# Optimization experiments

Hardware: AMD Instinct MI355X
Metric: run time of the kernel (lower is better)

## Reference

```python
import jax, jax.numpy as jnp
import numpy as np

N_PER_G = 100  # nodes per graph


def setup_inputs() -> dict:
    key = jax.random.key(0)
    ks = jax.random.split(key, 12)
    N, G, E = 100000, 1000, 1600000
    ninp, nout, K, H, H2 = 3, 10, 5, 64, 32
    x = jax.random.normal(ks[0], (N, ninp), jnp.float32)
    # within-graph random edges (contiguous node blocks per graph)
    epg = E // G
    gid = jnp.arange(E, dtype=jnp.int32) // epg
    src = jax.random.randint(ks[1], (E,), 0, N_PER_G, jnp.int32) + gid * N_PER_G
    dst = jax.random.randint(ks[2], (E,), 0, N_PER_G, jnp.int32) + gid * N_PER_G
    edge_index = jnp.stack([src, dst])
    batch = (jnp.arange(N, dtype=jnp.int32) // N_PER_G)
    lambda_max = 1.5 + 0.5 * jax.random.uniform(ks[3], (G,), jnp.float32)
    s = 0.05
    W1 = jax.random.normal(ks[4], (K, ninp, H), jnp.float32) * s
    b1 = jnp.zeros((H,), jnp.float32)
    W2 = jax.random.normal(ks[5], (K, H, H), jnp.float32) * s
    b2 = jnp.zeros((H,), jnp.float32)
    W3 = jax.random.normal(ks[6], (K, H, H), jnp.float32) * s
    b3 = jnp.zeros((H,), jnp.float32)
    bn_gamma = jnp.ones((H,), jnp.float32)
    bn_beta = jnp.zeros((H,), jnp.float32)
    bn_mean = jnp.zeros((H,), jnp.float32)
    bn_var = jnp.ones((H,), jnp.float32)
    fc1_w = jax.random.normal(ks[7], (H, H2), jnp.float32) * s
    fc1_b = jnp.zeros((H2,), jnp.float32)
    fc2_w = jax.random.normal(ks[8], (H2, nout), jnp.float32) * s
    fc2_b = jnp.zeros((nout,), jnp.float32)
    return dict(x=x, edge_index=edge_index, batch=batch, lambda_max=lambda_max,
                W1=W1, b1=b1, W2=W2, b2=b2, W3=W3, b3=b3,
                bn_gamma=bn_gamma, bn_beta=bn_beta, bn_mean=bn_mean, bn_var=bn_var,
                fc1_w=fc1_w, fc1_b=fc1_b, fc2_w=fc2_w, fc2_b=fc2_b)


def _cheb_conv(x, W, b, row, col, coef_edge, coef_loop):
    # PyG ChebConv with sym-normalized scaled Laplacian:
    # Lhat x = scatter_add(coef_edge * x[col] -> row) + coef_loop * x
    N = x.shape[0]
    def lhat(h):
        return jax.ops.segment_sum(coef_edge[:, None] * h[col], row,
                                   num_segments=N) + coef_loop[:, None] * h
    Tx0 = x
    out = Tx0 @ W[0]
    Tx1 = lhat(x)
    out = out + Tx1 @ W[1]
    for k in range(2, W.shape[0]):
        Tx2 = 2.0 * lhat(Tx1) - Tx0
        out = out + Tx2 @ W[k]
        Tx0, Tx1 = Tx1, Tx2
    return out + b


def reference(x, edge_index, batch, lambda_max,
              W1, b1, W2, b2, W3, b3,
              bn_gamma, bn_beta, bn_mean, bn_var,
              fc1_w, fc1_b, fc2_w, fc2_b):
    N = x.shape[0]
    G = lambda_max.shape[0]
    row, col = edge_index[0], edge_index[1]
    # sym Laplacian normalization, scaled by 2/lambda_max (per-graph)
    deg = jax.ops.segment_sum(jnp.ones_like(row, dtype=x.dtype), row, num_segments=N)
    dis = jnp.where(deg > 0, deg, 1.0) ** -0.5
    dis = jnp.where(deg > 0, dis, 0.0)
    lmax_e = lambda_max[batch[row]]
    coef_edge = -(2.0 / lmax_e) * dis[row] * dis[col]   # off-diagonal of Lhat
    coef_loop = 2.0 / lambda_max[batch] - 1.0           # diagonal of Lhat
    h = jax.nn.relu(_cheb_conv(x, W1, b1, row, col, coef_edge, coef_loop))
    h = jax.nn.relu(_cheb_conv(h, W2, b2, row, col, coef_edge, coef_loop))
    h = jax.nn.relu(_cheb_conv(h, W3, b3, row, col, coef_edge, coef_loop))
    # global mean pool over graphs
    sums = jax.ops.segment_sum(h, batch, num_segments=G)
    cnts = jax.ops.segment_sum(jnp.ones((N,), h.dtype), batch, num_segments=G)
    g = sums / jnp.maximum(cnts, 1.0)[:, None]
    # BatchNorm1d (eval mode, running stats), eps=1e-5
    g = (g - bn_mean) * jax.lax.rsqrt(bn_var + 1e-5) * bn_gamma + bn_beta
    g = jax.nn.relu(g @ fc1_w + fc1_b)
    return jax.nn.log_softmax(g @ fc2_w + fc2_b, axis=1)
```

## Files before the change

kernel.cpp:

```cpp
#include <hip/hip_runtime.h>

#define NPG 100
#define HF 64
#define NROW 128
#define ST 72
#define SAT 136
#define CMW 28

typedef float  f4   __attribute__((ext_vector_type(4)));
typedef float  f16v __attribute__((ext_vector_type(16)));
typedef short  bf8  __attribute__((ext_vector_type(8)));

#define SZ_TC  (HF * SAT * 2)
#define SZ_TRM (NROW * ST * 2)
#define OFF_TC  0
#define OFF_TRM SZ_TC
#define OFF_CM  0
#define OFF_MISC (OFF_TRM + SZ_TRM)
#define SMEM_BYTES (OFF_MISC + 1280)

#define WT_TOTAL 46080

__device__ __forceinline__ unsigned short f2bf(float f) {
    unsigned u = __float_as_uint(f);
    u += 0x7fffu + ((u >> 16) & 1u);
    return (unsigned short)(u >> 16);
}
__device__ __forceinline__ unsigned cvt_pk_bf16(float lo, float hi) {
    unsigned r;
    asm("v_cvt_pk_bf16_f32 %0, %1, %2" : "=v"(r) : "v"(lo), "v"(hi));
    return r;
}
__device__ __forceinline__ f16v zerov16() {
    f16v z;
    #pragma unroll
    for (int i = 0; i < 16; i++) z[i] = 0.f;
    return z;
}

union BF8U { unsigned u[4]; bf8 b; };

__global__ void wconv(const float* __restrict__ W1, const float* __restrict__ W2,
                      const float* __restrict__ W3, unsigned short* __restrict__ ws)
{
    int idx = blockIdx.x * 256 + threadIdx.x;
    if (idx >= WT_TOTAL) return;
    float v;
    if (idx < 5120) {
        int k5 = idx >> 10, rem = idx & 1023, fo = rem >> 4, fi = rem & 15;
        v = (fi < 3) ? W1[(k5 * 3 + fi) * HF + fo] : 0.f;
    } else if (idx < 25600) {
        int j = idx - 5120;
        int k5 = j >> 12, rem = j & 4095, fo = rem >> 6, fi = rem & 63;
        v = W2[(k5 * HF + fi) * HF + fo];
    } else {
        int j = idx - 25600;
        int k5 = j >> 12, rem = j & 4095, fo = rem >> 6, fi = rem & 63;
        v = W3[(k5 * HF + fi) * HF + fo];
    }
    ws[idx] = f2bf(v);
}

__launch_bounds__(256, 2)
__global__ void chebreg(const float* __restrict__ x, const int* __restrict__ ei,
                        const float* __restrict__ lambda_max,
                        const unsigned short* __restrict__ Wt,
                        const float* __restrict__ b1, const float* __restrict__ b2,
                        const float* __restrict__ b3,
                        const float* __restrict__ bng, const float* __restrict__ bnb,
                        const float* __restrict__ bnm, const float* __restrict__ bnv,
                        const float* __restrict__ fc1w, const float* __restrict__ fc1b,
                        const float* __restrict__ fc2w, const float* __restrict__ fc2b,
                        float* __restrict__ out, int E_total, int epg)
{
    extern __shared__ char sm[];
    const int tid = threadIdx.x;
    const int g = blockIdx.x;
    const int ebase = g * epg, nbase = g * NPG;
    const int wg = tid >> 6, lane = tid & 63;
    const int l31 = lane & 31, hh = lane >> 5;
    const int ht  = wg & 1;
    const int Mt0 = (wg >> 1) * 2;
    const int fo  = ht * 32 + l31;

    unsigned* Cm  = (unsigned*)(sm + OFF_CM);
    float* dis    = (float*)(sm + OFF_MISC);
    float* pool   = (float*)(sm + OFF_MISC + 448);
    float* gvn    = (float*)(sm + OFF_MISC + 704);
    float* zf     = (float*)(sm + OFF_MISC + 960);
    float* logits = (float*)(sm + OFF_MISC + 1088);
    float* lsep   = (float*)(sm + OFF_MISC + 1152);

    const float lam = lambda_max[g];
    const float two_l = 2.0f / lam;
    const float cl = two_l - 1.0f;

    for (int i = tid; i < (NROW * CMW) / 4; i += 256)
        ((f4*)Cm)[i] = (f4){0.f, 0.f, 0.f, 0.f};
    __syncthreads();
    for (int e = tid; e < epg; e += 256) {
        int r = ei[ebase + e] - nbase;
        int c = ei[E_total + ebase + e] - nbase;
        atomicAdd(&Cm[r * CMW + (c >> 2)], 1u << (8 * (c & 3)));
    }
    __syncthreads();
    if (tid < 112) {
        float dv = 0.f;
        if (tid < NPG) {
            unsigned s = 0;
            #pragma unroll
            for (int w = 0; w < CMW; w++) {
                unsigned u = Cm[tid * CMW + w];
                s += (u & 255) + ((u >> 8) & 255) + ((u >> 16) & 255) + (u >> 24);
            }
            dv = s > 0 ? rsqrtf((float)s) : 0.f;
        }
        dis[tid] = dv;
    }
    __syncthreads();

    bf8 af[2][7];
    #pragma unroll
    for (int m = 0; m < 2; m++) {
        int rr = 32 * (Mt0 + m) + l31;
        bool rv = (rr < NPG);
        float base = rv ? (-two_l * dis[rr]) : 0.f;
        #pragma unroll
        for (int Ks = 0; Ks < 7; Ks++) {
            int k0 = Ks * 16 + 8 * hh;
            unsigned w0 = rv ? Cm[rr * CMW + (k0 >> 2)]     : 0u;
            unsigned w1 = rv ? Cm[rr * CMW + (k0 >> 2) + 1] : 0u;
            float vv[8];
            #pragma unroll
            for (int j = 0; j < 8; j++) {
                int k = k0 + j;
                unsigned cnt = (((j < 4) ? w0 : w1) >> (8 * (k & 3))) & 255u;
                float v = base * (float)cnt * dis[k];
                if (rv && k == rr) v += cl;
                vv[j] = v;
            }
            BF8U t;
            #pragma unroll
            for (int p = 0; p < 4; p++) t.u[p] = cvt_pk_bf16(vv[2 * p], vv[2 * p + 1]);
            af[m][Ks] = t.b;
        }
    }
    __syncthreads();

    for (int i = tid; i < (SZ_TC + SZ_TRM) / 16; i += 256)
        ((f4*)sm)[i] = (f4){0.f, 0.f, 0.f, 0.f};
    if (tid < HF) pool[tid] = 0.f;
    __syncthreads();
    if (tid < NPG) {
        unsigned short h0 = f2bf(x[(nbase + tid) * 3 + 0]);
        unsigned short h1 = f2bf(x[(nbase + tid) * 3 + 1]);
        unsigned short h2 = f2bf(x[(nbase + tid) * 3 + 2]);
        *(unsigned*)(sm + OFF_TRM + (tid * ST) * 2) = (unsigned)h0 | ((unsigned)h1 << 16);
        *(unsigned short*)(sm + OFF_TRM + (tid * ST + 2) * 2) = h2;
        *(unsigned short*)(sm + OFF_TC + (0 * SAT + tid) * 2) = h0;
        *(unsigned short*)(sm + OFF_TC + (1 * SAT + tid) * 2) = h1;
        *(unsigned short*)(sm + OFF_TC + (2 * SAT + tid) * 2) = h2;
    }
    __syncthreads();

    f16v acc[2];
    unsigned prev[2][8], oldr[2][8];
    const float* bsv[3] = {b1, b2, b3};

    for (int L = 0; L < 3; L++) {
        const bool l1 = (L == 0);
        const unsigned short* Wl = l1 ? Wt : (Wt + (L == 1 ? 5120 : 25600));
        acc[0] = zerov16();
        acc[1] = zerov16();

        if (L == 0) {
            #pragma unroll
            for (int m = 0; m < 2; m++) {
                unsigned short tv[16];
                #pragma unroll
                for (int r = 0; r < 16; r++) {
                    int np = (Mt0 + m) * 32 + (r & 3) + 8 * (r >> 2) + 4 * hh;
                    tv[r] = *(const unsigned short*)(sm + OFF_TRM + (np * ST + fo) * 2);
                }
                #pragma unroll
                for (int p = 0; p < 8; p++)
                    prev[m][p] = (unsigned)tv[2 * p] | ((unsigned)tv[2 * p + 1] << 16);
            }
        }

        auto TW = [&](int k5) {
            const int nKs = l1 ? 1 : 4;
            for (int Ks = 0; Ks < nKs; Ks++) {
                bf8 bw;
                if (l1) bw = *(const bf8*)(Wl + (k5 * 64 + fo) * 16 + 8 * hh);
                else    bw = *(const bf8*)(Wl + (k5 * 64 + fo) * 64 + Ks * 16 + 8 * hh);
                #pragma unroll
                for (int m = 0; m < 2; m++) {
                    bf8 a = *(const bf8*)(sm + OFF_TRM +
                              (((Mt0 + m) * 32 + l31) * ST + Ks * 16 + 8 * hh) * 2);
                    acc[m] = __builtin_amdgcn_mfma_f32_32x32x16_bf16(a, bw, acc[m], 0, 0, 0);
                }
            }
        };

        TW(0);
        for (int s = 1; s <= 4; s++) {
            bf8 bfr[7];
            #pragma unroll
            for (int Ks = 0; Ks < 7; Ks++)
                bfr[Ks] = *(const bf8*)(sm + OFF_TC +
                            (fo * SAT + Ks * 16 + 8 * hh) * 2);
            __syncthreads();
            #pragma unroll
            for (int m = 0; m < 2; m++) {
                f16v c = zerov16();
                #pragma unroll
                for (int Ks = 0; Ks < 7; Ks++)
                    c = __builtin_amdgcn_mfma_f32_32x32x16_bf16(af[m][Ks], bfr[Ks], c, 0, 0, 0);
                #pragma unroll
                for (int p = 0; p < 8; p++) {
                    float ve = c[2 * p], vo = c[2 * p + 1];
                    if (s >= 2) {
                        unsigned o = oldr[m][p];
                        ve = 2.f * ve - __uint_as_float(o << 16);
                        vo = 2.f * vo - __uint_as_float(o & 0xffff0000u);
                    }
                    oldr[m][p] = prev[m][p];
                    prev[m][p] = cvt_pk_bf16(ve, vo);
                }
                #pragma unroll
                for (int q4 = 0; q4 < 4; q4++) {
                    int np0 = (Mt0 + m) * 32 + 8 * q4 + 4 * hh;
                    uint2 pk;
                    pk.x = prev[m][2 * q4];
                    pk.y = prev[m][2 * q4 + 1];
                    *(uint2*)(sm + OFF_TC + (fo * SAT + np0) * 2) = pk;
                }
                #pragma unroll
                for (int p = 0; p < 8; p++) {
                    int r0 = 2 * p;
                    int npb = (Mt0 + m) * 32 + (r0 & 3) + 8 * (r0 >> 2) + 4 * hh;
                    char* ad = sm + OFF_TRM + (npb * ST + fo) * 2;
                    *(unsigned short*)ad = (unsigned short)prev[m][p];
                    *(unsigned short*)(ad + ST * 2) = (unsigned short)(prev[m][p] >> 16);
                }
            }
            __syncthreads();
            TW(s);
        }
        __syncthreads();

        const float bias = bsv[L][fo];
        if (L < 2) {
            #pragma unroll
            for (int m = 0; m < 2; m++) {
                #pragma unroll
                for (int p = 0; p < 8; p++) {
                    float ve = fmaxf(acc[m][2 * p]     + bias, 0.f);
                    float vo = fmaxf(acc[m][2 * p + 1] + bias, 0.f);
                    prev[m][p] = cvt_pk_bf16(ve, vo);
                }
                #pragma unroll
                for (int q4 = 0; q4 < 4; q4++) {
                    int np0 = (Mt0 + m) * 32 + 8 * q4 + 4 * hh;
                    uint2 pk;
                    pk.x = prev[m][2 * q4];
                    pk.y = prev[m][2 * q4 + 1];
                    *(uint2*)(sm + OFF_TC + (fo * SAT + np0) * 2) = pk;
                }
                #pragma unroll
                for (int p = 0; p < 8; p++) {
                    int r0 = 2 * p;
                    int npb = (Mt0 + m) * 32 + (r0 & 3) + 8 * (r0 >> 2) + 4 * hh;
                    char* ad = sm + OFF_TRM + (npb * ST + fo) * 2;
                    *(unsigned short*)ad = (unsigned short)prev[m][p];
                    *(unsigned short*)(ad + ST * 2) = (unsigned short)(prev[m][p] >> 16);
                }
            }
            __syncthreads();
        } else {
            float ssum = 0.f;
            #pragma unroll
            for (int m = 0; m < 2; m++) {
                #pragma unroll
                for (int r = 0; r < 16; r++) {
                    int np = (Mt0 + m) * 32 + (r & 3) + 8 * (r >> 2) + 4 * hh;
                    float h = fmaxf(acc[m][r] + bias, 0.f);
                    if (np < NPG) ssum += h;
                }
            }
            ssum += __shfl_xor(ssum, 32, 64);
            if (hh == 0) atomicAdd(&pool[fo], ssum);
            __syncthreads();
        }
    }

    if (tid < HF) {
        float gv = pool[tid] * (1.0f / NPG);
        gv = (gv - bnm[tid]) * rsqrtf(bnv[tid] + 1e-5f) * bng[tid] + bnb[tid];
        gvn[tid] = gv;
    }
    __syncthreads();
    if (tid < 32) {
        float a = fc1b[tid];
        for (int f = 0; f < HF; f++) a += gvn[f] * fc1w[f * 32 + tid];
        zf[tid] = fmaxf(a, 0.f);
    }
    __syncthreads();
    if (tid < 10) {
        float a = fc2b[tid];
        for (int k = 0; k < 32; k++) a += zf[k] * fc2w[k * 10 + tid];
        logits[tid] = a;
    }
    __syncthreads();
    if (tid == 0) {
        float m = logits[0];
        for (int i = 1; i < 10; i++) m = fmaxf(m, logits[i]);
        float s = 0.f;
        for (int i = 0; i < 10; i++) s += expf(logits[i] - m);
        lsep[0] = m + logf(s);
    }
    __syncthreads();
    if (tid < 10) out[g * 10 + tid] = logits[tid] - lsep[0];
}

extern "C" void kernel_launch(void* const* d_in, const int* in_sizes, int n_in,
                              void* d_out, int out_size, void* d_ws, size_t ws_size,
                              hipStream_t stream) {
    const float* x    = (const float*)d_in[0];
    const int*   ei   = (const int*)d_in[1];
    const float* lmax = (const float*)d_in[3];
    const float* W1   = (const float*)d_in[4];
    const float* b1   = (const float*)d_in[5];
    const float* W2   = (const float*)d_in[6];
    const float* b2   = (const float*)d_in[7];
    const float* W3   = (const float*)d_in[8];
    const float* b3   = (const float*)d_in[9];
    const float* bng  = (const float*)d_in[10];
    const float* bnb  = (const float*)d_in[11];
    const float* bnm  = (const float*)d_in[12];
    const float* bnv  = (const float*)d_in[13];
    const float* fc1w = (const float*)d_in[14];
    const float* fc1b = (const float*)d_in[15];
    const float* fc2w = (const float*)d_in[16];
    const float* fc2b = (const float*)d_in[17];

    const int E = in_sizes[1] / 2;
    const int G = in_sizes[3];
    const int epg = E / G;

    unsigned short* Wt = (unsigned short*)d_ws;

    wconv<<<(WT_TOTAL + 255) / 256, 256, 0, stream>>>(W1, W2, W3, Wt);

    hipFuncSetAttribute((const void*)chebreg,
                        hipFuncAttributeMaxDynamicSharedMemorySize, SMEM_BYTES);

    chebreg<<<G, 256, SMEM_BYTES, stream>>>(x, ei, lmax, Wt, b1, b2, b3,
                                            bng, bnb, bnm, bnv, fc1w, fc1b, fc2w, fc2b,
                                            (float*)d_out, E, epg);
}
```

Before: 164.2 us.

## Restructure Chebyshev recurrence to node-major waves with register-resident T operands

Each wave now owns a 32-node slab and computes Lhat·T in transposed form, keeping the resulting T_k tiles in registers and feeding them to the weight MFMA through v_permlane32_swap. This drops the second row-major LDS copy of T. The T buffer is double-buffered so only one barrier is needed per recurrence step, and layer 1 skips the unused 32-feature half. Biases are staged in LDS, and pooling is a plain LDS reduction instead of atomics. The cost is more register pressure, two-byte scattered LDS stores, and a larger LDS footprint from the double buffer, which could reduce occupancy.

```diff
diff --git a/kernel.cpp b/kernel.cpp
--- a/kernel.cpp
+++ b/kernel.cpp
@@ -2,22 +2,17 @@
 
 #define NPG 100
 #define HF 64
-#define NROW 128
-#define ST 72
 #define SAT 136
-#define CMW 28
+#define CMW 29
 
 typedef float  f4   __attribute__((ext_vector_type(4)));
 typedef float  f16v __attribute__((ext_vector_type(16)));
 typedef short  bf8  __attribute__((ext_vector_type(8)));
 
-#define SZ_TC  (HF * SAT * 2)
-#define SZ_TRM (NROW * ST * 2)
-#define OFF_TC  0
-#define OFF_TRM SZ_TC
-#define OFF_CM  0
-#define OFF_MISC (OFF_TRM + SZ_TRM)
-#define SMEM_BYTES (OFF_MISC + 1280)
+#define NB_T  (HF * SAT * 2)
+#define OFF_MISC (2 * NB_T)
+#define MISC_BYTES 2048
+#define SMEM_BYTES (OFF_MISC + MISC_BYTES)
 
 #define WT_TOTAL 46080
 
@@ -79,23 +74,23 @@
     const int ebase = g * epg, nbase = g * NPG;
     const int wg = tid >> 6, lane = tid & 63;
     const int l31 = lane & 31, hh = lane >> 5;
-    const int ht  = wg & 1;
-    const int Mt0 = (wg >> 1) * 2;
-    const int fo  = ht * 32 + l31;
-
-    unsigned* Cm  = (unsigned*)(sm + OFF_CM);
+    const int nb = 32 * wg;
+    const int np = nb + l31;
+    const bool npv = (np < NPG);
+
+    unsigned* Cm  = (unsigned*)sm;
     float* dis    = (float*)(sm + OFF_MISC);
-    float* pool   = (float*)(sm + OFF_MISC + 448);
-    float* gvn    = (float*)(sm + OFF_MISC + 704);
-    float* zf     = (float*)(sm + OFF_MISC + 960);
-    float* logits = (float*)(sm + OFF_MISC + 1088);
-    float* lsep   = (float*)(sm + OFF_MISC + 1152);
+    float* b_all  = (float*)(sm + OFF_MISC + 448);
+    float* gvn    = (float*)(sm + OFF_MISC + 1216);
+    float* zf     = (float*)(sm + OFF_MISC + 1472);
+    float* logits = (float*)(sm + OFF_MISC + 1600);
+    float* lsep   = (float*)(sm + OFF_MISC + 1664);
 
     const float lam = lambda_max[g];
     const float two_l = 2.0f / lam;
     const float cl = two_l - 1.0f;
 
-    for (int i = tid; i < (NROW * CMW) / 4; i += 256)
+    for (int i = tid; i < (128 * CMW) / 4; i += 256)
         ((f4*)Cm)[i] = (f4){0.f, 0.f, 0.f, 0.f};
     __syncthreads();
     for (int e = tid; e < epg; e += 256) {
@@ -109,7 +104,7 @@
         if (tid < NPG) {
             unsigned s = 0;
             #pragma unroll
-            for (int w = 0; w < CMW; w++) {
+            for (int w = 0; w < 25; w++) {
                 unsigned u = Cm[tid * CMW + w];
                 s += (u & 255) + ((u >> 8) & 255) + ((u >> 16) & 255) + (u >> 24);
             }
@@ -117,190 +112,213 @@
         }
         dis[tid] = dv;
     }
-    __syncthreads();
-
-    bf8 af[2][7];
-    #pragma unroll
-    for (int m = 0; m < 2; m++) {
-        int rr = 32 * (Mt0 + m) + l31;
-        bool rv = (rr < NPG);
-        float base = rv ? (-two_l * dis[rr]) : 0.f;
+    if (tid < 192)
+        b_all[tid] = (tid < 64) ? b1[tid] : (tid < 128) ? b2[tid - 64] : b3[tid - 128];
+    __syncthreads();
+
+    bf8 afT[7];
+    {
+        float base = npv ? (-two_l * dis[np]) : 0.f;
         #pragma unroll
         for (int Ks = 0; Ks < 7; Ks++) {
-            int k0 = Ks * 16 + 8 * hh;
-            unsigned w0 = rv ? Cm[rr * CMW + (k0 >> 2)]     : 0u;
-            unsigned w1 = rv ? Cm[rr * CMW + (k0 >> 2) + 1] : 0u;
+            int n0 = Ks * 16 + 8 * hh;
+            unsigned w0 = npv ? Cm[np * CMW + (n0 >> 2)]     : 0u;
+            unsigned w1 = npv ? Cm[np * CMW + (n0 >> 2) + 1] : 0u;
             float vv[8];
             #pragma unroll
             for (int j = 0; j < 8; j++) {
-                int k = k0 + j;
-                unsigned cnt = (((j < 4) ? w0 : w1) >> (8 * (k & 3))) & 255u;
-                float v = base * (float)cnt * dis[k];
-                if (rv && k == rr) v += cl;
+                int n = n0 + j;
+                unsigned cnt = (((j < 4) ? w0 : w1) >> (8 * (n & 3))) & 255u;
+                float v = base * (float)cnt * dis[n];
+                if (npv && n == np) v += cl;
                 vv[j] = v;
             }
             BF8U t;
             #pragma unroll
             for (int p = 0; p < 4; p++) t.u[p] = cvt_pk_bf16(vv[2 * p], vv[2 * p + 1]);
-            af[m][Ks] = t.b;
+            afT[Ks] = t.b;
         }
     }
     __syncthreads();
 
-    for (int i = tid; i < (SZ_TC + SZ_TRM) / 16; i += 256)
+    for (int i = tid; i < (2 * NB_T) / 16; i += 256)
         ((f4*)sm)[i] = (f4){0.f, 0.f, 0.f, 0.f};
-    if (tid < HF) pool[tid] = 0.f;
-    __syncthreads();
-    if (tid < NPG) {
-        unsigned short h0 = f2bf(x[(nbase + tid) * 3 + 0]);
-        unsigned short h1 = f2bf(x[(nbase + tid) * 3 + 1]);
-        unsigned short h2 = f2bf(x[(nbase + tid) * 3 + 2]);
-        *(unsigned*)(sm + OFF_TRM + (tid * ST) * 2) = (unsigned)h0 | ((unsigned)h1 << 16);
-        *(unsigned short*)(sm + OFF_TRM + (tid * ST + 2) * 2) = h2;
-        *(unsigned short*)(sm + OFF_TC + (0 * SAT + tid) * 2) = h0;
-        *(unsigned short*)(sm + OFF_TC + (1 * SAT + tid) * 2) = h1;
-        *(unsigned short*)(sm + OFF_TC + (2 * SAT + tid) * 2) = h2;
+    __syncthreads();
+
+    unsigned prev[2][8], oldr[2][8];
+    #pragma unroll
+    for (int ct = 0; ct < 2; ct++)
+        #pragma unroll
+        for (int p = 0; p < 8; p++) prev[ct][p] = 0u;
+
+    if (hh == 0 && npv) {
+        float x0 = x[(nbase + np) * 3 + 0];
+        float x1 = x[(nbase + np) * 3 + 1];
+        float x2 = x[(nbase + np) * 3 + 2];
+        prev[0][0] = cvt_pk_bf16(x0, x1);
+        prev[0][1] = cvt_pk_bf16(x2, 0.f);
+        *(unsigned short*)(sm + (0 * SAT + np) * 2) = (unsigned short)(prev[0][0] & 0xffff);
+        *(unsigned short*)(sm + (1 * SAT + np) * 2) = (unsigned short)(prev[0][0] >> 16);
+        *(unsigned short*)(sm + (2 * SAT + np) * 2) = (unsigned short)(prev[0][1] & 0xffff);
     }
     __syncthreads();
 
     f16v acc[2];
-    unsigned prev[2][8], oldr[2][8];
-    const float* bsv[3] = {b1, b2, b3};
+    int cur = 0;
 
     for (int L = 0; L < 3; L++) {
-        const bool l1 = (L == 0);
-        const unsigned short* Wl = l1 ? Wt : (Wt + (L == 1 ? 5120 : 25600));
+        const bool l0 = (L == 0);
+        const unsigned short* Wl = l0 ? Wt : (Wt + (L == 1 ? 5120 : 25600));
+        const int wstr = l0 ? 16 : 64;
+        const int nKs  = l0 ? 1 : 4;
         acc[0] = zerov16();
         acc[1] = zerov16();
 
-        if (L == 0) {
-            #pragma unroll
-            for (int m = 0; m < 2; m++) {
-                unsigned short tv[16];
-                #pragma unroll
-                for (int r = 0; r < 16; r++) {
-                    int np = (Mt0 + m) * 32 + (r & 3) + 8 * (r >> 2) + 4 * hh;
-                    tv[r] = *(const unsigned short*)(sm + OFF_TRM + (np * ST + fo) * 2);
-                }
-                #pragma unroll
-                for (int p = 0; p < 8; p++)
-                    prev[m][p] = (unsigned)tv[2 * p] | ((unsigned)tv[2 * p + 1] << 16);
-            }
-        }
-
-        auto TW = [&](int k5) {
-            const int nKs = l1 ? 1 : 4;
-            for (int Ks = 0; Ks < nKs; Ks++) {
-                bf8 bw;
-                if (l1) bw = *(const bf8*)(Wl + (k5 * 64 + fo) * 16 + 8 * hh);
-                else    bw = *(const bf8*)(Wl + (k5 * 64 + fo) * 64 + Ks * 16 + 8 * hh);
-                #pragma unroll
-                for (int m = 0; m < 2; m++) {
-                    bf8 a = *(const bf8*)(sm + OFF_TRM +
-                              (((Mt0 + m) * 32 + l31) * ST + Ks * 16 + 8 * hh) * 2);
-                    acc[m] = __builtin_amdgcn_mfma_f32_32x32x16_bf16(a, bw, acc[m], 0, 0, 0);
+        auto TWreg = [&](int k5) {
+            #pragma unroll
+            for (int Ks = 0; Ks < 4; Ks++) {
+                if (Ks < nKs) {
+                    unsigned a0 = prev[Ks >> 1][4 * (Ks & 1) + 0];
+                    unsigned b0 = prev[Ks >> 1][4 * (Ks & 1) + 2];
+                    unsigned a1 = prev[Ks >> 1][4 * (Ks & 1) + 1];
+                    unsigned b1v = prev[Ks >> 1][4 * (Ks & 1) + 3];
+                    asm volatile("v_permlane32_swap_b32 %0, %1" : "+v"(a0), "+v"(b0));
+                    asm volatile("v_permlane32_swap_b32 %0, %1" : "+v"(a1), "+v"(b1v));
+                    BF8U bfr; bfr.u[0] = a0; bfr.u[1] = a1; bfr.u[2] = b0; bfr.u[3] = b1v;
+                    #pragma unroll
+                    for (int ct = 0; ct < 2; ct++) {
+                        bf8 wf = *(const bf8*)(Wl + (k5 * 64 + 32 * ct + l31) * wstr
+                                               + Ks * 16 + 8 * hh);
+                        acc[ct] = __builtin_amdgcn_mfma_f32_32x32x16_bf16(wf, bfr.b, acc[ct], 0, 0, 0);
+                    }
                 }
             }
         };
 
-        TW(0);
         for (int s = 1; s <= 4; s++) {
-            bf8 bfr[7];
+            const char* bcur = sm + cur * NB_T;
+            bf8 Af0[7], Af1[7];
             #pragma unroll
             for (int Ks = 0; Ks < 7; Ks++)
-                bfr[Ks] = *(const bf8*)(sm + OFF_TC +
-                            (fo * SAT + Ks * 16 + 8 * hh) * 2);
-            __syncthreads();
-            #pragma unroll
-            for (int m = 0; m < 2; m++) {
-                f16v c = zerov16();
+                Af0[Ks] = *(const bf8*)(bcur + ((0 + l31) * SAT + Ks * 16 + 8 * hh) * 2);
+            if (!l0) {
                 #pragma unroll
                 for (int Ks = 0; Ks < 7; Ks++)
-                    c = __builtin_amdgcn_mfma_f32_32x32x16_bf16(af[m][Ks], bfr[Ks], c, 0, 0, 0);
+                    Af1[Ks] = *(const bf8*)(bcur + ((32 + l31) * SAT + Ks * 16 + 8 * hh) * 2);
+            }
+            f16v c0 = zerov16(), c1 = zerov16();
+            #pragma unroll
+            for (int Ks = 0; Ks < 7; Ks++)
+                c0 = __builtin_amdgcn_mfma_f32_32x32x16_bf16(Af0[Ks], afT[Ks], c0, 0, 0, 0);
+            if (!l0) {
+                #pragma unroll
+                for (int Ks = 0; Ks < 7; Ks++)
+                    c1 = __builtin_amdgcn_mfma_f32_32x32x16_bf16(Af1[Ks], afT[Ks], c1, 0, 0, 0);
+            }
+
+            TWreg(s - 1);
+
+            #pragma unroll
+            for (int p = 0; p < 8; p++) {
+                float ve = c0[2 * p], vo = c0[2 * p + 1];
+                if (s >= 2) {
+                    unsigned o = oldr[0][p];
+                    ve = 2.f * ve - __uint_as_float(o << 16);
+                    vo = 2.f * vo - __uint_as_float(o & 0xffff0000u);
+                }
+                oldr[0][p] = prev[0][p];
+                prev[0][p] = cvt_pk_bf16(ve, vo);
+            }
+            if (!l0) {
                 #pragma unroll
                 for (int p = 0; p < 8; p++) {
-                    float ve = c[2 * p], vo = c[2 * p + 1];
+                    float ve = c1[2 * p], vo = c1[2 * p + 1];
                     if (s >= 2) {
-                        unsigned o = oldr[m][p];
+                        unsigned o = oldr[1][p];
                         ve = 2.f * ve - __uint_as_float(o << 16);
                         vo = 2.f * vo - __uint_as_float(o & 0xffff0000u);
                     }
-                    oldr[m][p] = prev[m][p];
-                    prev[m][p] = cvt_pk_bf16(ve, vo);
-                }
-                #pragma unroll
-                for (int q4 = 0; q4 < 4; q4++) {
-                    int np0 = (Mt0 + m) * 32 + 8 * q4 + 4 * hh;
-                    uint2 pk;
-                    pk.x = prev[m][2 * q4];
-                    pk.y = prev[m][2 * q4 + 1];
-                    *(uint2*)(sm + OFF_TC + (fo * SAT + np0) * 2) = pk;
-                }
+                    oldr[1][p] = prev[1][p];
+                    prev[1][p] = cvt_pk_bf16(ve, vo);
+                }
+            }
+
+            if (s < 4) {
+                char* bnx = sm + (cur ^ 1) * NB_T;
+                if (l0) {
+                    if (hh == 0) {
+                        *(unsigned short*)(bnx + (0 * SAT + np) * 2) = (unsigned short)(prev[0][0] & 0xffff);
+                        *(unsigned short*)(bnx + (1 * SAT + np) * 2) = (unsigned short)(prev[0][0] >> 16);
+                        *(unsigned short*)(bnx + (2 * SAT + np) * 2) = (unsigned short)(prev[0][1] & 0xffff);
+                    }
+                } else {
+                    #pragma unroll
+                    for (int ct = 0; ct < 2; ct++) {
+                        #pragma unroll
+                        for (int p = 0; p < 8; p++) {
+                            int fo = 32 * ct + ((2 * p) & 3) + 8 * (p >> 1) + 4 * hh;
+                            *(unsigned short*)(bnx + (fo * SAT + np) * 2)       = (unsigned short)(prev[ct][p] & 0xffff);
+                            *(unsigned short*)(bnx + ((fo + 1) * SAT + np) * 2) = (unsigned short)(prev[ct][p] >> 16);
+                        }
+                    }
+                }
+            }
+            __syncthreads();
+            cur ^= 1;
+        }
+
+        TWreg(4);
+
+        if (L < 2) {
+            const float* bl = b_all + L * 64;
+            char* bt0 = sm + cur * NB_T;
+            #pragma unroll
+            for (int ct = 0; ct < 2; ct++) {
                 #pragma unroll
                 for (int p = 0; p < 8; p++) {
-                    int r0 = 2 * p;
-                    int npb = (Mt0 + m) * 32 + (r0 & 3) + 8 * (r0 >> 2) + 4 * hh;
-                    char* ad = sm + OFF_TRM + (npb * ST + fo) * 2;
-                    *(unsigned short*)ad = (unsigned short)prev[m][p];
-                    *(unsigned short*)(ad + ST * 2) = (unsigned short)(prev[m][p] >> 16);
-                }
-            }
-            __syncthreads();
-            TW(s);
-        }
-        __syncthreads();
-
-        const float bias = bsv[L][fo];
-        if (L < 2) {
-            #pragma unroll
-            for (int m = 0; m < 2; m++) {
-                #pragma unroll
-                for (int p = 0; p < 8; p++) {
-                    float ve = fmaxf(acc[m][2 * p]     + bias, 0.f);
-                    float vo = fmaxf(acc[m][2 * p + 1] + bias, 0.f);
-                    prev[m][p] = cvt_pk_bf16(ve, vo);
-                }
-                #pragma unroll
-                for (int q4 = 0; q4 < 4; q4++) {
-                    int np0 = (Mt0 + m) * 32 + 8 * q4 + 4 * hh;
-                    uint2 pk;
-                    pk.x = prev[m][2 * q4];
-                    pk.y = prev[m][2 * q4 + 1];
-                    *(uint2*)(sm + OFF_TC + (fo * SAT + np0) * 2) = pk;
-                }
-                #pragma unroll
-                for (int p = 0; p < 8; p++) {
-                    int r0 = 2 * p;
-                    int npb = (Mt0 + m) * 32 + (r0 & 3) + 8 * (r0 >> 2) + 4 * hh;
-                    char* ad = sm + OFF_TRM + (npb * ST + fo) * 2;
-                    *(unsigned short*)ad = (unsigned short)prev[m][p];
-                    *(unsigned short*)(ad + ST * 2) = (unsigned short)(prev[m][p] >> 16);
+                    int fo = 32 * ct + ((2 * p) & 3) + 8 * (p >> 1) + 4 * hh;
+                    float2 bb = *(const float2*)(bl + fo);
+                    float ve = fmaxf(acc[ct][2 * p]     + bb.x, 0.f);
+                    float vo = fmaxf(acc[ct][2 * p + 1] + bb.y, 0.f);
+                    prev[ct][p] = cvt_pk_bf16(ve, vo);
+                    *(unsigned short*)(bt0 + (fo * SAT + np) * 2)       = (unsigned short)(prev[ct][p] & 0xffff);
+                    *(unsigned short*)(bt0 + ((fo + 1) * SAT + np) * 2) = (unsigned short)(prev[ct][p] >> 16);
                 }
             }
             __syncthreads();
         } else {
-            float ssum = 0.f;
-            #pragma unroll
-            for (int m = 0; m < 2; m++) {
-                #pragma unroll
-                for (int r = 0; r < 16; r++) {
-                    int np = (Mt0 + m) * 32 + (r & 3) + 8 * (r >> 2) + 4 * hh;
-                    float h = fmaxf(acc[m][r] + bias, 0.f);
-                    if (np < NPG) ssum += h;
-                }
-            }
-            ssum += __shfl_xor(ssum, 32, 64);
-            if (hh == 0) atomicAdd(&pool[fo], ssum);
+            float* Sc = (float*)sm;
+            const float* bl = b_all + 128;
+            #pragma unroll
+            for (int ct = 0; ct < 2; ct++) {
+                #pragma unroll
+                for (int p = 0; p < 8; p++) {
+                    int fo = 32 * ct + ((2 * p) & 3) + 8 * (p >> 1) + 4 * hh;
+                    float2 bb = *(const float2*)(bl + fo);
+                    float ve = fmaxf(acc[ct][2 * p]     + bb.x, 0.f);
+                    float vo = fmaxf(acc[ct][2 * p + 1] + bb.y, 0.f);
+                    if (npv) {
+                        Sc[fo * 132 + np]       = ve;
+                        Sc[(fo + 1) * 132 + np] = vo;
+                    }
+                }
+            }
+            __syncthreads();
+            if (tid < HF) {
+                float ssum = 0.f;
+                #pragma unroll
+                for (int k = 0; k < 25; k++) {
+                    f4 v = *(const f4*)(Sc + tid * 132 + 4 * k);
+                    ssum += v[0] + v[1] + v[2] + v[3];
+                }
+                float gv = ssum * (1.0f / NPG);
+                gv = (gv - bnm[tid]) * rsqrtf(bnv[tid] + 1e-5f) * bng[tid] + bnb[tid];
+                gvn[tid] = gv;
+            }
             __syncthreads();
         }
     }
 
-    if (tid < HF) {
-        float gv = pool[tid] * (1.0f / NPG);
-        gv = (gv - bnm[tid]) * rsqrtf(bnv[tid] + 1e-5f) * bng[tid] + bnb[tid];
-        gvn[tid] = gv;
-    }
-    __syncthreads();
     if (tid < 32) {
         float a = fc1b[tid];
         for (int f = 0; f < HF; f++) a += gvn[f] * fc1w[f * 32 + tid];
```

After: 181.5 us. 1.11x slower.

## Double-buffer Chebyshev LDS tiles to drop one barrier per recurrence step

Applied to the files above, without the earlier changes.

Splits the transposed and row-major bf16 feature tiles into two ping-pong LDS buffers, so each Chebyshev step reads one buffer and writes the next. This removes the barrier that separated the reads from the overwrites. The weight-multiply of the previous term now runs before the Laplacian product inside the same step. All __syncthreads are replaced by a custom LDS-wait-plus-s_barrier with a scheduling fence. The edge-count matrix row stride changes to 29 words to cut bank conflicts. LDS use grows to roughly double the feature-tile footprint, which may lower occupancy.

```diff
diff --git a/kernel.cpp b/kernel.cpp
--- a/kernel.cpp
+++ b/kernel.cpp
@@ -2,21 +2,18 @@
 
 #define NPG 100
 #define HF 64
-#define NROW 128
 #define ST 72
 #define SAT 136
-#define CMW 28
+#define CMW 29
 
 typedef float  f4   __attribute__((ext_vector_type(4)));
 typedef float  f16v __attribute__((ext_vector_type(16)));
 typedef short  bf8  __attribute__((ext_vector_type(8)));
 
 #define SZ_TC  (HF * SAT * 2)
-#define SZ_TRM (NROW * ST * 2)
-#define OFF_TC  0
-#define OFF_TRM SZ_TC
-#define OFF_CM  0
-#define OFF_MISC (OFF_TRM + SZ_TRM)
+#define SZ_TRM (128 * ST * 2)
+#define OFF_TRM (2 * SZ_TC)
+#define OFF_MISC (OFF_TRM + 2 * SZ_TRM)
 #define SMEM_BYTES (OFF_MISC + 1280)
 
 #define WT_TOTAL 46080
@@ -36,6 +33,11 @@
     #pragma unroll
     for (int i = 0; i < 16; i++) z[i] = 0.f;
     return z;
+}
+__device__ __forceinline__ void bar_lgkm() {
+    asm volatile("s_waitcnt lgkmcnt(0)" ::: "memory");
+    __builtin_amdgcn_s_barrier();
+    __builtin_amdgcn_sched_barrier(0);
 }
 
 union BF8U { unsigned u[4]; bf8 b; };
@@ -83,7 +85,7 @@
     const int Mt0 = (wg >> 1) * 2;
     const int fo  = ht * 32 + l31;
 
-    unsigned* Cm  = (unsigned*)(sm + OFF_CM);
+    unsigned* Cm  = (unsigned*)sm;
     float* dis    = (float*)(sm + OFF_MISC);
     float* pool   = (float*)(sm + OFF_MISC + 448);
     float* gvn    = (float*)(sm + OFF_MISC + 704);
@@ -95,21 +97,21 @@
     const float two_l = 2.0f / lam;
     const float cl = two_l - 1.0f;
 
-    for (int i = tid; i < (NROW * CMW) / 4; i += 256)
+    for (int i = tid; i < (128 * CMW) / 4; i += 256)
         ((f4*)Cm)[i] = (f4){0.f, 0.f, 0.f, 0.f};
-    __syncthreads();
+    bar_lgkm();
     for (int e = tid; e < epg; e += 256) {
         int r = ei[ebase + e] - nbase;
         int c = ei[E_total + ebase + e] - nbase;
         atomicAdd(&Cm[r * CMW + (c >> 2)], 1u << (8 * (c & 3)));
     }
-    __syncthreads();
+    bar_lgkm();
     if (tid < 112) {
         float dv = 0.f;
         if (tid < NPG) {
             unsigned s = 0;
             #pragma unroll
-            for (int w = 0; w < CMW; w++) {
+            for (int w = 0; w < 25; w++) {
                 unsigned u = Cm[tid * CMW + w];
                 s += (u & 255) + ((u >> 8) & 255) + ((u >> 16) & 255) + (u >> 24);
             }
@@ -117,7 +119,7 @@
         }
         dis[tid] = dv;
     }
-    __syncthreads();
+    bar_lgkm();
 
     bf8 af[2][7];
     #pragma unroll
@@ -145,23 +147,25 @@
             af[m][Ks] = t.b;
         }
     }
-    __syncthreads();
-
-    for (int i = tid; i < (SZ_TC + SZ_TRM) / 16; i += 256)
+    bar_lgkm();
+
+    for (int i = tid; i < SZ_TC / 16; i += 256)
         ((f4*)sm)[i] = (f4){0.f, 0.f, 0.f, 0.f};
+    for (int i = tid; i < SZ_TRM / 16; i += 256)
+        ((f4*)(sm + OFF_TRM))[i] = (f4){0.f, 0.f, 0.f, 0.f};
     if (tid < HF) pool[tid] = 0.f;
-    __syncthreads();
+    bar_lgkm();
     if (tid < NPG) {
         unsigned short h0 = f2bf(x[(nbase + tid) * 3 + 0]);
         unsigned short h1 = f2bf(x[(nbase + tid) * 3 + 1]);
         unsigned short h2 = f2bf(x[(nbase + tid) * 3 + 2]);
         *(unsigned*)(sm + OFF_TRM + (tid * ST) * 2) = (unsigned)h0 | ((unsigned)h1 << 16);
         *(unsigned short*)(sm + OFF_TRM + (tid * ST + 2) * 2) = h2;
-        *(unsigned short*)(sm + OFF_TC + (0 * SAT + tid) * 2) = h0;
-        *(unsigned short*)(sm + OFF_TC + (1 * SAT + tid) * 2) = h1;
-        *(unsigned short*)(sm + OFF_TC + (2 * SAT + tid) * 2) = h2;
-    }
-    __syncthreads();
+        *(unsigned short*)(sm + (0 * SAT + tid) * 2) = h0;
+        *(unsigned short*)(sm + (1 * SAT + tid) * 2) = h1;
+        *(unsigned short*)(sm + (2 * SAT + tid) * 2) = h2;
+    }
+    bar_lgkm();
 
     f16v acc[2];
     unsigned prev[2][8], oldr[2][8];
@@ -170,6 +174,8 @@
     for (int L = 0; L < 3; L++) {
         const bool l1 = (L == 0);
         const unsigned short* Wl = l1 ? Wt : (Wt + (L == 1 ? 5120 : 25600));
+        const int pb = L & 1;
+        const float bias = bsv[L][fo];
         acc[0] = zerov16();
         acc[1] = zerov16();
 
@@ -188,7 +194,7 @@
             }
         }
 
-        auto TW = [&](int k5) {
+        auto TW = [&](int k5, const char* trb) {
             const int nKs = l1 ? 1 : 4;
             for (int Ks = 0; Ks < nKs; Ks++) {
                 bf8 bw;
@@ -196,21 +202,27 @@
                 else    bw = *(const bf8*)(Wl + (k5 * 64 + fo) * 64 + Ks * 16 + 8 * hh);
                 #pragma unroll
                 for (int m = 0; m < 2; m++) {
-                    bf8 a = *(const bf8*)(sm + OFF_TRM +
+                    bf8 a = *(const bf8*)(trb +
                               (((Mt0 + m) * 32 + l31) * ST + Ks * 16 + 8 * hh) * 2);
                     acc[m] = __builtin_amdgcn_mfma_f32_32x32x16_bf16(a, bw, acc[m], 0, 0, 0);
                 }
             }
         };
 
-        TW(0);
         for (int s = 1; s <= 4; s++) {
+            const int rp = (pb + s - 1) & 1, wp = rp ^ 1;
+            const char* tcR = sm + rp * SZ_TC;
+            const char* trR = sm + OFF_TRM + rp * SZ_TRM;
+            char* tcW = sm + wp * SZ_TC;
+            char* trW = sm + OFF_TRM + wp * SZ_TRM;
+
+            TW(s - 1, trR);
+
             bf8 bfr[7];
             #pragma unroll
             for (int Ks = 0; Ks < 7; Ks++)
-                bfr[Ks] = *(const bf8*)(sm + OFF_TC +
-                            (fo * SAT + Ks * 16 + 8 * hh) * 2);
-            __syncthreads();
+                bfr[Ks] = *(const bf8*)(tcR + (fo * SAT + Ks * 16 + 8 * hh) * 2);
+
             #pragma unroll
             for (int m = 0; m < 2; m++) {
                 f16v c = zerov16();
@@ -228,56 +240,60 @@
                     oldr[m][p] = prev[m][p];
                     prev[m][p] = cvt_pk_bf16(ve, vo);
                 }
+                if (s < 4) {
+                    #pragma unroll
+                    for (int q4 = 0; q4 < 4; q4++) {
+                        int np0 = (Mt0 + m) * 32 + 8 * q4 + 4 * hh;
+                        uint2 pk;
+                        pk.x = prev[m][2 * q4];
+                        pk.y = prev[m][2 * q4 + 1];
+                        *(uint2*)(tcW + (fo * SAT + np0) * 2) = pk;
+                    }
+                }
+                #pragma unroll
+                for (int p = 0; p < 8; p++) {
+                    int r0 = 2 * p;
+                    int npb = (Mt0 + m) * 32 + (r0 & 3) + 8 * (r0 >> 2) + 4 * hh;
+                    char* ad = trW + (npb * ST + fo) * 2;
+                    *(unsigned short*)ad = (unsigned short)prev[m][p];
+                    *(unsigned short*)(ad + ST * 2) = (unsigned short)(prev[m][p] >> 16);
+                }
+            }
+            bar_lgkm();
+        }
+
+        TW(4, sm + OFF_TRM + pb * SZ_TRM);
+
+        if (L < 2) {
+            const int op = pb ^ 1;
+            char* tcW = sm + op * SZ_TC;
+            char* trW = sm + OFF_TRM + op * SZ_TRM;
+            #pragma unroll
+            for (int m = 0; m < 2; m++) {
+                #pragma unroll
+                for (int p = 0; p < 8; p++) {
+                    float ve = fmaxf(acc[m][2 * p]     + bias, 0.f);
+                    float vo = fmaxf(acc[m][2 * p + 1] + bias, 0.f);
+                    prev[m][p] = cvt_pk_bf16(ve, vo);
+                }
                 #pragma unroll
                 for (int q4 = 0; q4 < 4; q4++) {
                     int np0 = (Mt0 + m) * 32 + 8 * q4 + 4 * hh;
                     uint2 pk;
                     pk.x = prev[m][2 * q4];
                     pk.y = prev[m][2 * q4 + 1];
-                    *(uint2*)(sm + OFF_TC + (fo * SAT + np0) * 2) = pk;
+                    *(uint2*)(tcW + (fo * SAT + np0) * 2) = pk;
                 }
                 #pragma unroll
                 for (int p = 0; p < 8; p++) {
                     int r0 = 2 * p;
                     int npb = (Mt0 + m) * 32 + (r0 & 3) + 8 * (r0 >> 2) + 4 * hh;
-                    char* ad = sm + OFF_TRM + (npb * ST + fo) * 2;
+                    char* ad = trW + (npb * ST + fo) * 2;
                     *(unsigned short*)ad = (unsigned short)prev[m][p];
                     *(unsigned short*)(ad + ST * 2) = (unsigned short)(prev[m][p] >> 16);
                 }
             }
-            __syncthreads();
-            TW(s);
-        }
-        __syncthreads();
-
-        const float bias = bsv[L][fo];
-        if (L < 2) {
-            #pragma unroll
-            for (int m = 0; m < 2; m++) {
-                #pragma unroll
-                for (int p = 0; p < 8; p++) {
-                    float ve = fmaxf(acc[m][2 * p]     + bias, 0.f);
-                    float vo = fmaxf(acc[m][2 * p + 1] + bias, 0.f);
-                    prev[m][p] = cvt_pk_bf16(ve, vo);
-                }
-                #pragma unroll
-                for (int q4 = 0; q4 < 4; q4++) {
-                    int np0 = (Mt0 + m) * 32 + 8 * q4 + 4 * hh;
-                    uint2 pk;
-                    pk.x = prev[m][2 * q4];
-                    pk.y = prev[m][2 * q4 + 1];
-                    *(uint2*)(sm + OFF_TC + (fo * SAT + np0) * 2) = pk;
-                }
-                #pragma unroll
-                for (int p = 0; p < 8; p++) {
-                    int r0 = 2 * p;
-                    int npb = (Mt0 + m) * 32 + (r0 & 3) + 8 * (r0 >> 2) + 4 * hh;
-                    char* ad = sm + OFF_TRM + (npb * ST + fo) * 2;
-                    *(unsigned short*)ad = (unsigned short)prev[m][p];
-                    *(unsigned short*)(ad + ST * 2) = (unsigned short)(prev[m][p] >> 16);
-                }
-            }
-            __syncthreads();
+            bar_lgkm();
         } else {
             float ssum = 0.f;
             #pragma unroll
@@ -291,7 +307,7 @@
             }
             ssum += __shfl_xor(ssum, 32, 64);
             if (hh == 0) atomicAdd(&pool[fo], ssum);
-            __syncthreads();
+            bar_lgkm();
         }
     }
 
@@ -300,19 +316,19 @@
         gv = (gv - bnm[tid]) * rsqrtf(bnv[tid] + 1e-5f) * bng[tid] + bnb[tid];
         gvn[tid] = gv;
     }
-    __syncthreads();
+    bar_lgkm();
     if (tid < 32) {
         float a = fc1b[tid];
         for (int f = 0; f < HF; f++) a += gvn[f] * fc1w[f * 32 + tid];
         zf[tid] = fmaxf(a, 0.f);
     }
-    __syncthreads();
+    bar_lgkm();
     if (tid < 10) {
         float a = fc2b[tid];
         for (int k = 0; k < 32; k++) a += zf[k] * fc2w[k * 10 + tid];
         logits[tid] = a;
     }
-    __syncthreads();
+    bar_lgkm();
     if (tid == 0) {
         float m = logits[0];
         for (int i = 1; i < 10; i++) m = fmaxf(m, logits[i]);
@@ -320,7 +336,7 @@
         for (int i = 0; i < 10; i++) s += expf(logits[i] - m);
         lsep[0] = m + logf(s);
     }
-    __syncthreads();
+    bar_lgkm();
     if (tid < 10) out[g * 10 + tid] = logits[tid] - lsep[0];
 }
 
```

Result: faster. 159.5 us (-2.8%).
